# Kernel optimization log

Hardware: AMD Instinct MI355X
Metric: run time of the kernel (lower is better)

Reference implementation:

```python
import jax, jax.numpy as jnp
import numpy as np

_DIMS = [15, 30, 60, 90, 120, 90, 60, 30, 15, 10, 5, 1]


def setup_inputs() -> dict:
    key = jax.random.key(0)
    keys = jax.random.split(key, 1 + 2 * 11)
    inp = {"x": jax.random.normal(keys[0], (524288, 15), dtype=jnp.float32)}
    for i in range(11):
        fan_in, fan_out = _DIMS[i], _DIMS[i + 1]
        bound = 1.0 / np.sqrt(fan_in)
        inp[f"W{i+1}"] = jax.random.uniform(keys[1 + 2 * i], (fan_out, fan_in), minval=-bound, maxval=bound, dtype=jnp.float32)
        inp[f"b{i+1}"] = jax.random.uniform(keys[2 + 2 * i], (fan_out,), minval=-bound, maxval=bound, dtype=jnp.float32)
    return inp


def reference(x, W1, b1, W2, b2, W3, b3, W4, b4, W5, b5, W6, b6, W7, b7, W8, b8, W9, b9, W10, b10, W11, b11):
    Ws = [W1, W2, W3, W4, W5, W6, W7, W8, W9, W10, W11]
    bs = [b1, b2, b3, b4, b5, b6, b7, b8, b9, b10, b11]
    h = x
    # 10 Linear+ReLU layers, funnel 15->30->60->90->120->90->60->30->15->10->5
    for W, b in zip(Ws[:-1], bs[:-1]):
        h = jax.nn.relu(h @ W.T + b)
    # final Linear 5->1 + sigmoid
    return jax.nn.sigmoid(h @ Ws[-1].T + bs[-1])
```

## Files before the change

### kernel.cpp

```cpp
#include <hip/hip_runtime.h>
#include <math.h>


using bf16x8 = __attribute__((ext_vector_type(8))) short;
using f32x4  = __attribute__((ext_vector_type(4))) float;
using u16x8  = __attribute__((ext_vector_type(8))) unsigned short;
using u32x2  = __attribute__((ext_vector_type(2))) unsigned;
using u32x4  = __attribute__((ext_vector_type(4))) unsigned;
typedef __bf16 bf16x2_t __attribute__((ext_vector_type(2)));

namespace {
constexpr int NL = 11;
constexpr int IN_[NL]  = {15, 30, 60, 90, 120, 90, 60, 30, 15, 10, 5};
constexpr int OUT_[NL] = {30, 60, 90, 120, 90, 60, 30, 15, 10, 5, 1};
constexpr int KP_[NL]  = {32, 32, 64, 96, 128, 96, 64, 32, 32, 32, 32};
constexpr int NP_[NL]  = {32, 64, 96, 128, 96, 64, 32, 16, 16, 16, 16};
constexpr int E0 = 0;
constexpr int E1 = 1024;
constexpr int E2 = 5120;
constexpr int E3 = 11264;
constexpr int E4 = 19456;
constexpr int E5 = 25600;
constexpr int LDS_SHORTS = 29696;
constexpr int LDS_BYTES  = LDS_SHORTS * 2;
constexpr int G = 32;
}

__device__ __forceinline__ unsigned short f2bf(float f) {
    unsigned u = __float_as_uint(f);
    u += 0x7fffu + ((u >> 16) & 1u);
    return (unsigned short)(u >> 16);
}

__device__ __forceinline__ unsigned pk2(float a, float b) {
#if __has_builtin(__builtin_amdgcn_cvt_pk_bf16_f32)
    return __builtin_bit_cast(unsigned, __builtin_amdgcn_cvt_pk_bf16_f32(a, b));
#else
    bf16x2_t c;
    c[0] = (__bf16)a;
    c[1] = (__bf16)b;
    return __builtin_bit_cast(unsigned, c);
#endif
}

__device__ __forceinline__ u32x2 packrelu(f32x4 a) {
    u32x2 p;
    p[0] = pk2(fmaxf(a[0], 0.f), fmaxf(a[1], 0.f));
    p[1] = pk2(fmaxf(a[2], 0.f), fmaxf(a[3], 0.f));
    return p;
}

__device__ __forceinline__ bf16x8 xform(u32x2 pa, u32x2 pb, bool sel, int sA, int sB) {
    int a0 = __shfl((int)pa[0], sA);
    int b0 = __shfl((int)pb[0], sA);
    int a1 = __shfl((int)pa[1], sA);
    int b1 = __shfl((int)pb[1], sA);
    int a2 = __shfl((int)pa[0], sB);
    int b2 = __shfl((int)pb[0], sB);
    int a3 = __shfl((int)pa[1], sB);
    int b3 = __shfl((int)pb[1], sB);
    u32x4 r;
    r[0] = (unsigned)(sel ? b0 : a0);
    r[1] = (unsigned)(sel ? b1 : a1);
    r[2] = (unsigned)(sel ? b2 : a2);
    r[3] = (unsigned)(sel ? b3 : a3);
    return __builtin_bit_cast(bf16x8, r);
}

__device__ __forceinline__ bf16x8 xform16(u32x2 p, int quad, int sA16, int sB16) {
    int d0 = __shfl((int)p[0], sA16);
    int d1 = __shfl((int)p[1], sA16);
    int d2 = __shfl((int)p[0], sB16);
    int d3 = __shfl((int)p[1], sB16);
    u32x4 r;
    if (quad < 2) {
        r[0] = (unsigned)d0; r[1] = (unsigned)d1;
        r[2] = (unsigned)d2; r[3] = (unsigned)d3;
    } else {
        r[0] = (quad == 2) ? 0x00003F80u : 0u;
        r[1] = 0u; r[2] = 0u; r[3] = 0u;
    }
    return __builtin_bit_cast(bf16x8, r);
}

template <int L>
__device__ __forceinline__ void stage_w(const float* __restrict__ W,
                                        const float* __restrict__ B,
                                        short* s, int tid) {
    constexpr int KP = KP_[L], NP = NP_[L], INl = IN_[L], OUTl = OUT_[L];
    constexpr int NKT = KP / 32;
    for (int idx = tid; idx < NP * KP; idx += 512) {
        const int f    = idx >> 9;
        const int t    = idx & 511;
        const int quad = t >> 7;
        const int colc = (t >> 3) & 15;
        const int j    = t & 7;
        const int mt   = f / NKT;
        const int kt   = f - mt * NKT;
        const int m    = mt * 16 + colc;
        const int k    = kt * 32 + quad * 8 + j;
        float v = 0.f;
        if (m < OUTl) {
            if (k < INl) v = W[m * INl + k];
            else if (k == INl) v = B[m];
            else if (k == INl + 1) {
                float hf = __builtin_bit_cast(float, (unsigned)f2bf(B[m]) << 16);
                v = B[m] - hf;
            }
        } else if (m == OUTl || m == OUTl + 1) {
            if (k == INl) v = 1.f;
        }
        s[idx] = (short)f2bf(v);
    }
}

__device__ __forceinline__ bf16x8 ldfrag(const short* p) { return *(const bf16x8*)p; }

__device__ __forceinline__ void edge_write(short* tile, int mt, int col, int quad, f32x4 a) {
    const int wb = (mt >> 1) * 512 + ((mt & 1) * 2 + (quad >> 1)) * 128 + col * 8 + (quad & 1) * 4;
    *(u32x2*)(tile + wb) = packrelu(a);
}

__device__ __forceinline__ float4 ld4(const float* p) {
    float4 t;
    __builtin_memcpy(&t, p, 16);
    return t;
}

__device__ __forceinline__ void fetch_x2(const float* __restrict__ x, int row0,
                                         int col, int quad, float4 (&xv)[2]) {
#pragma unroll
    for (int t = 0; t < 2; ++t) {
        const float* xr = x + (long)(row0 + t * 16 + col) * 15;
        if (quad < 3) {
            xv[t] = ld4(xr + quad * 4);
        } else {
            float4 u = ld4(xr + 11);
            xv[t] = make_float4(u.y, u.z, u.w, 1.f);
        }
    }
}

extern "C" __global__ void __launch_bounds__(512, 4)
mlp_pipe(const float* __restrict__ x,
         const float* __restrict__ W0,  const float* __restrict__ B0,
         const float* __restrict__ W1,  const float* __restrict__ B1,
         const float* __restrict__ W2,  const float* __restrict__ B2,
         const float* __restrict__ W3,  const float* __restrict__ B3,
         const float* __restrict__ W4,  const float* __restrict__ B4,
         const float* __restrict__ W5,  const float* __restrict__ B5,
         const float* __restrict__ W6,  const float* __restrict__ B6,
         const float* __restrict__ W7,  const float* __restrict__ B7,
         const float* __restrict__ W8,  const float* __restrict__ B8,
         const float* __restrict__ W9,  const float* __restrict__ B9,
         const float* __restrict__ W10, const float* __restrict__ B10,
         float* __restrict__ out, int ng) {
    extern __shared__ __align__(16) short smem[];
    const int tid  = threadIdx.x;
    const int wave = tid >> 6;
    const int lane = tid & 63;
    const int col  = lane & 15;
    const int quad = lane >> 4;
    const int fo   = quad * 128 + col * 8;
    const bool sel = quad >= 2;
    const int sA   = col + 16 * (2 * (quad & 1));
    const int sB   = sA + 16;
    const int sA16 = col + 32 * (quad & 1);
    const int sB16 = sA16 + 16;

    bf16x8 wreg[12];
#pragma unroll
    for (int f = 0; f < 12; ++f) wreg[f] = bf16x8{0,0,0,0,0,0,0,0};

    stage_w<0>(W0, B0, smem, tid); __syncthreads();
    if (wave == 0) { wreg[0] = ldfrag(smem + fo); wreg[1] = ldfrag(smem + 512 + fo); }
    __syncthreads();
    stage_w<1>(W1, B1, smem, tid); __syncthreads();
    if (wave == 0) {
#pragma unroll
        for (int f = 0; f < 4; ++f) wreg[2 + f] = ldfrag(smem + f * 512 + fo);
    }
    __syncthreads();
    stage_w<2>(W2, B2, smem, tid); __syncthreads();
    if (wave == 1) {
#pragma unroll
        for (int f = 0; f < 12; ++f) wreg[f] = ldfrag(smem + f * 512 + fo);
    }
    __syncthreads();
    stage_w<3>(W3, B3, smem, tid); __syncthreads();
    if (wave == 2) {
#pragma unroll
        for (int f = 0; f < 12; ++f) wreg[f] = ldfrag(smem + f * 512 + fo);
    }
    if (wave == 3) {
#pragma unroll
        for (int f = 0; f < 12; ++f) wreg[f] = ldfrag(smem + (12 + f) * 512 + fo);
    }
    __syncthreads();
    stage_w<4>(W4, B4, smem, tid); __syncthreads();
    if (wave == 4) {
#pragma unroll
        for (int f = 0; f < 12; ++f) wreg[f] = ldfrag(smem + f * 512 + fo);
    }
    if (wave == 5) {
#pragma unroll
        for (int f = 0; f < 12; ++f) wreg[f] = ldfrag(smem + (12 + f) * 512 + fo);
    }
    __syncthreads();
    stage_w<5>(W5, B5, smem, tid); __syncthreads();
    if (wave == 6) {
#pragma unroll
        for (int f = 0; f < 12; ++f) wreg[f] = ldfrag(smem + f * 512 + fo);
    }
    __syncthreads();
    stage_w<6>(W6, B6, smem, tid); __syncthreads();
    if (wave == 7) {
#pragma unroll
        for (int f = 0; f < 4; ++f) wreg[f] = ldfrag(smem + f * 512 + fo);
    }
    __syncthreads();
    stage_w<7>(W7, B7, smem, tid); __syncthreads();
    if (wave == 7) wreg[4] = ldfrag(smem + fo);
    __syncthreads();
    stage_w<8>(W8, B8, smem, tid); __syncthreads();
    if (wave == 7) wreg[5] = ldfrag(smem + fo);
    __syncthreads();
    stage_w<9>(W9, B9, smem, tid); __syncthreads();
    if (wave == 7) wreg[6] = ldfrag(smem + fo);
    __syncthreads();
    stage_w<10>(W10, B10, smem, tid); __syncthreads();
    if (wave == 7) wreg[7] = ldfrag(smem + fo);
    __syncthreads();

    const int gbase = blockIdx.x * ng;
    float4 xv[2];
    if (wave == 0 && ng > 0) fetch_x2(x, gbase * G, col, quad, xv);

    for (int n = 0; n < ng + 5; ++n) {
        if (wave == 0) {
            const int g = n;
            if (g < ng) {
                short* sx = smem + E0;
                const int off = (quad >> 1) * 128 + col * 8 + (quad & 1) * 4;
#pragma unroll
                for (int t = 0; t < 2; ++t) {
                    u32x2 o;
                    o[0] = pk2(xv[t].x, xv[t].y);
                    o[1] = pk2(xv[t].z, xv[t].w);
                    *(u32x2*)(sx + t * 512 + off) = o;
                }
                u16x8 z = {0, 0, 0, 0, 0, 0, 0, 0};
                if (!(quad & 1)) z[0] = (unsigned short)0x3F80;
                *(u16x8*)(sx + (quad >> 1) * 512 + (2 + (quad & 1)) * 128 + col * 8) = z;

                if (g + 1 < ng) fetch_x2(x, (gbase + g + 1) * G, col, quad, xv);

                short* e1p = smem + E1 + (g & 1) * 2048;
#pragma unroll
                for (int t = 0; t < 2; ++t) {
                    bf16x8 xb = ldfrag(sx + t * 512 + fo);
                    f32x4 a0 = {0.f, 0.f, 0.f, 0.f}, a1 = {0.f, 0.f, 0.f, 0.f};
                    a0 = __builtin_amdgcn_mfma_f32_16x16x32_bf16(wreg[0], xb, a0, 0, 0, 0);
                    a1 = __builtin_amdgcn_mfma_f32_16x16x32_bf16(wreg[1], xb, a1, 0, 0, 0);
                    bf16x8 h1 = xform(packrelu(a0), packrelu(a1), sel, sA, sB);
                    f32x4 c[4];
#pragma unroll
                    for (int mt = 0; mt < 4; ++mt) c[mt] = f32x4{0.f, 0.f, 0.f, 0.f};
#pragma unroll
                    for (int mt = 0; mt < 4; ++mt)
                        c[mt] = __builtin_amdgcn_mfma_f32_16x16x32_bf16(wreg[2 + mt], h1, c[mt], 0, 0, 0);
#pragma unroll
                    for (int mt = 0; mt < 4; ++mt)
                        edge_write(e1p + t * 1024, mt, col, quad, c[mt]);
                }
            }
        } else if (wave == 1) {
            const int g = n - 1;
            if (g >= 0 && g < ng) {
                const short* e1p = smem + E1 + (g & 1) * 2048;
                short* e2p = smem + E2 + (g & 1) * 3072;
#pragma unroll
                for (int t = 0; t < 2; ++t) {
                    bf16x8 b0 = ldfrag(e1p + t * 1024 + fo);
                    bf16x8 b1 = ldfrag(e1p + t * 1024 + 512 + fo);
                    f32x4 acc[6];
#pragma unroll
                    for (int mt = 0; mt < 6; ++mt) acc[mt] = f32x4{0.f, 0.f, 0.f, 0.f};
#pragma unroll
                    for (int mt = 0; mt < 6; ++mt)
                        acc[mt] = __builtin_amdgcn_mfma_f32_16x16x32_bf16(wreg[mt * 2], b0, acc[mt], 0, 0, 0);
#pragma unroll
                    for (int mt = 0; mt < 6; ++mt)
                        acc[mt] = __builtin_amdgcn_mfma_f32_16x16x32_bf16(wreg[mt * 2 + 1], b1, acc[mt], 0, 0, 0);
#pragma unroll
                    for (int mt = 0; mt < 6; ++mt)
                        edge_write(e2p + t * 1536, mt, col, quad, acc[mt]);
                }
            }
        } else if (wave == 2 || wave == 3) {
            const int g = n - 2;
            if (g >= 0 && g < ng) {
                const short* e2p = smem + E2 + (g & 1) * 3072;
                short* e3p = smem + E3 + (g & 1) * 4096;
                const int mo = (wave == 3) ? 4 : 0;
                f32x4 acc[4][2];
#pragma unroll
                for (int mt = 0; mt < 4; ++mt)
#pragma unroll
                    for (int t = 0; t < 2; ++t) acc[mt][t] = f32x4{0.f, 0.f, 0.f, 0.f};
#pragma unroll
                for (int kt = 0; kt < 3; ++kt) {
                    bf16x8 q0 = ldfrag(e2p + kt * 512 + fo);
                    bf16x8 q1 = ldfrag(e2p + 1536 + kt * 512 + fo);
#pragma unroll
                    for (int mt = 0; mt < 4; ++mt) {
                        acc[mt][0] = __builtin_amdgcn_mfma_f32_16x16x32_bf16(wreg[mt * 3 + kt], q0, acc[mt][0], 0, 0, 0);
                        acc[mt][1] = __builtin_amdgcn_mfma_f32_16x16x32_bf16(wreg[mt * 3 + kt], q1, acc[mt][1], 0, 0, 0);
                    }
                }
#pragma unroll
                for (int mt = 0; mt < 4; ++mt)
#pragma unroll
                    for (int t = 0; t < 2; ++t)
                        edge_write(e3p + t * 2048, mo + mt, col, quad, acc[mt][t]);
            }
        } else if (wave == 4 || wave == 5) {
            const int g = n - 3;
            if (g >= 0 && g < ng) {
                const short* e3p = smem + E3 + (g & 1) * 4096;
                short* e4p = smem + E4 + (g & 1) * 3072;
                const int mo = (wave == 5) ? 3 : 0;
                f32x4 acc[3][2];
#pragma unroll
                for (int mt = 0; mt < 3; ++mt)
#pragma unroll
                    for (int t = 0; t < 2; ++t) acc[mt][t] = f32x4{0.f, 0.f, 0.f, 0.f};
#pragma unroll
                for (int kt = 0; kt < 4; ++kt) {
                    bf16x8 q0 = ldfrag(e3p + kt * 512 + fo);
                    bf16x8 q1 = ldfrag(e3p + 2048 + kt * 512 + fo);
#pragma unroll
                    for (int mt = 0; mt < 3; ++mt) {
                        const int f = mt * 4 + kt + ((wave == 5) ? 12 - 12 : 0);
                        acc[mt][0] = __builtin_amdgcn_mfma_f32_16x16x32_bf16(wreg[f], q0, acc[mt][0], 0, 0, 0);
                        acc[mt][1] = __builtin_amdgcn_mfma_f32_16x16x32_bf16(wreg[f], q1, acc[mt][1], 0, 0, 0);
                    }
                }
#pragma unroll
                for (int mt = 0; mt < 3; ++mt)
#pragma unroll
                    for (int t = 0; t < 2; ++t)
                        edge_write(e4p + t * 1536, mo + mt, col, quad, acc[mt][t]);
            }
        } else if (wave == 6) {
            const int g = n - 4;
            if (g >= 0 && g < ng) {
                const short* e4p = smem + E4 + (g & 1) * 3072;
                short* e5p = smem + E5 + (g & 1) * 2048;
                f32x4 acc[4][2];
#pragma unroll
                for (int mt = 0; mt < 4; ++mt)
#pragma unroll
                    for (int t = 0; t < 2; ++t) acc[mt][t] = f32x4{0.f, 0.f, 0.f, 0.f};
#pragma unroll
                for (int kt = 0; kt < 3; ++kt) {
                    bf16x8 q0 = ldfrag(e4p + kt * 512 + fo);
                    bf16x8 q1 = ldfrag(e4p + 1536 + kt * 512 + fo);
#pragma unroll
                    for (int mt = 0; mt < 4; ++mt) {
                        acc[mt][0] = __builtin_amdgcn_mfma_f32_16x16x32_bf16(wreg[mt * 3 + kt], q0, acc[mt][0], 0, 0, 0);
                        acc[mt][1] = __builtin_amdgcn_mfma_f32_16x16x32_bf16(wreg[mt * 3 + kt], q1, acc[mt][1], 0, 0, 0);
                    }
                }
#pragma unroll
                for (int mt = 0; mt < 4; ++mt)
#pragma unroll
                    for (int t = 0; t < 2; ++t)
                        edge_write(e5p + t * 1024, mt, col, quad, acc[mt][t]);
            }
        } else {
            const int g = n - 5;
            if (g >= 0 && g < ng) {
                const short* e5p = smem + E5 + (g & 1) * 2048;
#pragma unroll
                for (int t = 0; t < 2; ++t) {
                    bf16x8 b0 = ldfrag(e5p + t * 1024 + fo);
                    bf16x8 b1 = ldfrag(e5p + t * 1024 + 512 + fo);
                    f32x4 c0 = {0.f, 0.f, 0.f, 0.f}, c1 = {0.f, 0.f, 0.f, 0.f};
                    c0 = __builtin_amdgcn_mfma_f32_16x16x32_bf16(wreg[0], b0, c0, 0, 0, 0);
                    c0 = __builtin_amdgcn_mfma_f32_16x16x32_bf16(wreg[1], b1, c0, 0, 0, 0);
                    c1 = __builtin_amdgcn_mfma_f32_16x16x32_bf16(wreg[2], b0, c1, 0, 0, 0);
                    c1 = __builtin_amdgcn_mfma_f32_16x16x32_bf16(wreg[3], b1, c1, 0, 0, 0);
                    bf16x8 h7 = xform(packrelu(c0), packrelu(c1), sel, sA, sB);
                    f32x4 d = {0.f, 0.f, 0.f, 0.f};
                    d = __builtin_amdgcn_mfma_f32_16x16x32_bf16(wreg[4], h7, d, 0, 0, 0);
                    bf16x8 h8 = xform16(packrelu(d), quad, sA16, sB16);
                    f32x4 e = {0.f, 0.f, 0.f, 0.f};
                    e = __builtin_amdgcn_mfma_f32_16x16x32_bf16(wreg[5], h8, e, 0, 0, 0);
                    bf16x8 h9 = xform16(packrelu(e), quad, sA16, sB16);
                    f32x4 ff = {0.f, 0.f, 0.f, 0.f};
                    ff = __builtin_amdgcn_mfma_f32_16x16x32_bf16(wreg[6], h9, ff, 0, 0, 0);
                    bf16x8 h10 = xform16(packrelu(ff), quad, sA16, sB16);
                    f32x4 o = {0.f, 0.f, 0.f, 0.f};
                    o = __builtin_amdgcn_mfma_f32_16x16x32_bf16(wreg[7], h10, o, 0, 0, 0);
                    if (quad == 0)
                        out[(gbase + g) * G + t * 16 + col] = 1.f / (1.f + __expf(-o[0]));
                }
            }
        }
        __syncthreads();
    }
}

extern "C" void kernel_launch(void* const* d_in, const int* in_sizes, int n_in,
                              void* d_out, int out_size, void* d_ws, size_t ws_size,
                              hipStream_t stream) {
    (void)n_in; (void)d_ws; (void)ws_size; (void)out_size;
    const float* x = (const float*)d_in[0];
    const float* W[11];
    const float* B[11];
    for (int i = 0; i < 11; ++i) {
        W[i] = (const float*)d_in[1 + 2 * i];
        B[i] = (const float*)d_in[2 + 2 * i];
    }
    const int nrows  = in_sizes[0] / 15;
    const int blocks = 512;
    const int ng     = (nrows / G) / blocks;

    hipFuncSetAttribute((const void*)mlp_pipe,
                        hipFuncAttributeMaxDynamicSharedMemorySize, LDS_BYTES);

    mlp_pipe<<<dim3(blocks), dim3(512), LDS_BYTES, stream>>>(
        x,
        W[0], B[0], W[1], B[1], W[2], B[2], W[3], B[3], W[4], B[4],
        W[5], B[5], W[6], B[6], W[7], B[7], W[8], B[8], W[9], B[9],
        W[10], B[10],
        (float*)d_out, ng);
}
```

Measured before the change: 212.6 us.

## Use 16x16x16 MFMA for small layers, drop shuffles, move x fetch to last wave

Narrow layers (first two and last four) now use the 16x16x16 bf16 MFMA, so activations go straight from the accumulator layout into the next B operand, with no cross-lane shuffle transforms. The x prefetch and conversion move from wave 0 to wave 7, which writes a double-buffered bf16 x tile in LDS one group ahead. Weight staging is consolidated into two phases with fewer barriers, and the launch bound changes from 4 to 2 blocks per CU. The aim is to shorten the critical first and last pipeline stages. The cost is extra LDS traffic for x and possible register or occupancy shifts.

After: 209.0 us. Within noise of the previous version (-1.7%).

```diff
diff --git a/kernel.cpp b/kernel.cpp
--- a/kernel.cpp
+++ b/kernel.cpp
@@ -3,10 +3,9 @@
 
 
 using bf16x8 = __attribute__((ext_vector_type(8))) short;
+using s16x4  = __attribute__((ext_vector_type(4))) short;
 using f32x4  = __attribute__((ext_vector_type(4))) float;
-using u16x8  = __attribute__((ext_vector_type(8))) unsigned short;
 using u32x2  = __attribute__((ext_vector_type(2))) unsigned;
-using u32x4  = __attribute__((ext_vector_type(4))) unsigned;
 typedef __bf16 bf16x2_t __attribute__((ext_vector_type(2)));
 
 namespace {
@@ -15,14 +14,17 @@
 constexpr int OUT_[NL] = {30, 60, 90, 120, 90, 60, 30, 15, 10, 5, 1};
 constexpr int KP_[NL]  = {32, 32, 64, 96, 128, 96, 64, 32, 32, 32, 32};
 constexpr int NP_[NL]  = {32, 64, 96, 128, 96, 64, 32, 16, 16, 16, 16};
-constexpr int E0 = 0;
-constexpr int E1 = 1024;
-constexpr int E2 = 5120;
-constexpr int E3 = 11264;
-constexpr int E4 = 19456;
-constexpr int E5 = 25600;
+constexpr int E1 = 0;
+constexpr int E2 = 4096;
+constexpr int E3 = 10240;
+constexpr int E4 = 18432;
+constexpr int E5 = 24576;
+constexpr int E6 = 28672;
 constexpr int LDS_SHORTS = 29696;
 constexpr int LDS_BYTES  = LDS_SHORTS * 2;
+constexpr int S_L0 = 0, S_L1 = 512, S_L2 = 2560, S_L3 = 8704;
+constexpr int S_L7 = 20992, S_L8 = 21504, S_L9 = 21760, S_L10 = 22016;
+constexpr int S_L4 = 0, S_L5 = 12288, S_L6 = 18432;
 constexpr int G = 32;
 }
 
@@ -33,12 +35,10 @@
 }
 
 __device__ __forceinline__ unsigned pk2(float a, float b) {
-#if __has_builtin(__builtin_amdgcn_cvt_pk_bf16_f32)
+#if defined(__HIP_DEVICE_COMPILE__) && __has_builtin(__builtin_amdgcn_cvt_pk_bf16_f32)
     return __builtin_bit_cast(unsigned, __builtin_amdgcn_cvt_pk_bf16_f32(a, b));
 #else
-    bf16x2_t c;
-    c[0] = (__bf16)a;
-    c[1] = (__bf16)b;
+    bf16x2_t c; c[0] = (__bf16)a; c[1] = (__bf16)b;
     return __builtin_bit_cast(unsigned, c);
 #endif
 }
@@ -49,44 +49,41 @@
     p[1] = pk2(fmaxf(a[2], 0.f), fmaxf(a[3], 0.f));
     return p;
 }
-
-__device__ __forceinline__ bf16x8 xform(u32x2 pa, u32x2 pb, bool sel, int sA, int sB) {
-    int a0 = __shfl((int)pa[0], sA);
-    int b0 = __shfl((int)pb[0], sA);
-    int a1 = __shfl((int)pa[1], sA);
-    int b1 = __shfl((int)pb[1], sA);
-    int a2 = __shfl((int)pa[0], sB);
-    int b2 = __shfl((int)pb[0], sB);
-    int a3 = __shfl((int)pa[1], sB);
-    int b3 = __shfl((int)pb[1], sB);
-    u32x4 r;
-    r[0] = (unsigned)(sel ? b0 : a0);
-    r[1] = (unsigned)(sel ? b1 : a1);
-    r[2] = (unsigned)(sel ? b2 : a2);
-    r[3] = (unsigned)(sel ? b3 : a3);
-    return __builtin_bit_cast(bf16x8, r);
-}
-
-__device__ __forceinline__ bf16x8 xform16(u32x2 p, int quad, int sA16, int sB16) {
-    int d0 = __shfl((int)p[0], sA16);
-    int d1 = __shfl((int)p[1], sA16);
-    int d2 = __shfl((int)p[0], sB16);
-    int d3 = __shfl((int)p[1], sB16);
-    u32x4 r;
-    if (quad < 2) {
-        r[0] = (unsigned)d0; r[1] = (unsigned)d1;
-        r[2] = (unsigned)d2; r[3] = (unsigned)d3;
-    } else {
-        r[0] = (quad == 2) ? 0x00003F80u : 0u;
-        r[1] = 0u; r[2] = 0u; r[3] = 0u;
-    }
-    return __builtin_bit_cast(bf16x8, r);
+__device__ __forceinline__ s16x4 pr16(f32x4 a) {
+    return __builtin_bit_cast(s16x4, packrelu(a));
+}
+
+__device__ __forceinline__ f32x4 mfma32(bf16x8 a, bf16x8 b, f32x4 c) {
+    return __builtin_amdgcn_mfma_f32_16x16x32_bf16(a, b, c, 0, 0, 0);
+}
+
+__device__ __forceinline__ s16x4 lo8(bf16x8 v) { return __builtin_shufflevector(v, v, 0, 1, 2, 3); }
+__device__ __forceinline__ s16x4 hi8(bf16x8 v) { return __builtin_shufflevector(v, v, 4, 5, 6, 7); }
+__device__ __forceinline__ bf16x8 cat4(s16x4 a, s16x4 b) { return __builtin_shufflevector(a, b, 0, 1, 2, 3, 4, 5, 6, 7); }
+
+__device__ __forceinline__ f32x4 mfma16(s16x4 a, s16x4 b, f32x4 c) {
+#if defined(__HIP_DEVICE_COMPILE__) && __has_builtin(__builtin_amdgcn_mfma_f32_16x16x16bf16_1k)
+    return __builtin_amdgcn_mfma_f32_16x16x16bf16_1k(a, b, c, 0, 0, 0);
+#else
+    const s16x4 z = {0, 0, 0, 0};
+    return mfma32(cat4(a, z), cat4(b, z), c);
+#endif
+}
+
+__device__ __forceinline__ bf16x8 ldfrag(const short* p) { return *(const bf16x8*)p; }
+__device__ __forceinline__ s16x4 ld16(const short* base, int f, int quad, int col) {
+    return *(const s16x4*)(base + f * 256 + quad * 64 + col * 4);
+}
+
+__device__ __forceinline__ void edge_write(short* tile, int mt, int col, int quad, f32x4 a) {
+    const int wb = (mt >> 1) * 512 + ((mt & 1) * 2 + (quad >> 1)) * 128 + col * 8 + (quad & 1) * 4;
+    *(u32x2*)(tile + wb) = packrelu(a);
 }
 
 template <int L>
 __device__ __forceinline__ void stage_w(const float* __restrict__ W,
                                         const float* __restrict__ B,
-                                        short* s, int tid) {
+                                        short* dst, int tid) {
     constexpr int KP = KP_[L], NP = NP_[L], INl = IN_[L], OUTl = OUT_[L];
     constexpr int NKT = KP / 32;
     for (int idx = tid; idx < NP * KP; idx += 512) {
@@ -110,21 +107,42 @@
         } else if (m == OUTl || m == OUTl + 1) {
             if (k == INl) v = 1.f;
         }
-        s[idx] = (short)f2bf(v);
-    }
-}
-
-__device__ __forceinline__ bf16x8 ldfrag(const short* p) { return *(const bf16x8*)p; }
-
-__device__ __forceinline__ void edge_write(short* tile, int mt, int col, int quad, f32x4 a) {
-    const int wb = (mt >> 1) * 512 + ((mt & 1) * 2 + (quad >> 1)) * 128 + col * 8 + (quad & 1) * 4;
-    *(u32x2*)(tile + wb) = packrelu(a);
+        dst[idx] = (short)f2bf(v);
+    }
+}
+
+template <int INl, int OUTl, int KP16, int NP, bool BLO, int NGEN>
+__device__ __forceinline__ void stage_w16(const float* __restrict__ W,
+                                          const float* __restrict__ B,
+                                          short* dst, int tid) {
+    for (int idx = tid; idx < NP * KP16; idx += 512) {
+        const int f    = idx >> 8;
+        const int t    = idx & 255;
+        const int quad = t >> 6;
+        const int colc = (t >> 2) & 15;
+        const int j    = t & 3;
+        constexpr int NKT = KP16 / 16;
+        const int mt   = f / NKT;
+        const int kt   = f - mt * NKT;
+        const int m    = mt * 16 + colc;
+        const int k    = kt * 16 + quad * 4 + j;
+        float v = 0.f;
+        if (m < OUTl) {
+            if (k < INl) v = W[m * INl + k];
+            else if (k == INl) v = B[m];
+            else if (BLO && k == INl + 1) {
+                float hf = __builtin_bit_cast(float, (unsigned)f2bf(B[m]) << 16);
+                v = B[m] - hf;
+            }
+        } else if (m < OUTl + NGEN) {
+            if (k == INl) v = 1.f;
+        }
+        dst[idx] = (short)f2bf(v);
+    }
 }
 
 __device__ __forceinline__ float4 ld4(const float* p) {
-    float4 t;
-    __builtin_memcpy(&t, p, 16);
-    return t;
+    float4 t; __builtin_memcpy(&t, p, 16); return t;
 }
 
 __device__ __forceinline__ void fetch_x2(const float* __restrict__ x, int row0,
@@ -141,7 +159,7 @@
     }
 }
 
-extern "C" __global__ void __launch_bounds__(512, 4)
+extern "C" __global__ void __launch_bounds__(512, 2)
 mlp_pipe(const float* __restrict__ x,
          const float* __restrict__ W0,  const float* __restrict__ B0,
          const float* __restrict__ W1,  const float* __restrict__ B1,
@@ -157,124 +175,108 @@
          float* __restrict__ out, int ng) {
     extern __shared__ __align__(16) short smem[];
     const int tid  = threadIdx.x;
-    const int wave = tid >> 6;
     const int lane = tid & 63;
     const int col  = lane & 15;
     const int quad = lane >> 4;
     const int fo   = quad * 128 + col * 8;
-    const bool sel = quad >= 2;
-    const int sA   = col + 16 * (2 * (quad & 1));
-    const int sB   = sA + 16;
-    const int sA16 = col + 32 * (quad & 1);
-    const int sB16 = sA16 + 16;
-
-    bf16x8 wreg[12];
-#pragma unroll
-    for (int f = 0; f < 12; ++f) wreg[f] = bf16x8{0,0,0,0,0,0,0,0};
-
-    stage_w<0>(W0, B0, smem, tid); __syncthreads();
-    if (wave == 0) { wreg[0] = ldfrag(smem + fo); wreg[1] = ldfrag(smem + 512 + fo); }
+    const int sw   = __builtin_amdgcn_readfirstlane(tid >> 6);
+
+    bf16x8 wk[12];
+#pragma unroll
+    for (int f = 0; f < 12; ++f) wk[f] = bf16x8{0, 0, 0, 0, 0, 0, 0, 0};
+    s16x4 t7a{0,0,0,0}, t7b{0,0,0,0}, t8{0,0,0,0}, t9{0,0,0,0}, t10{0,0,0,0};
+
+    stage_w16<15, 30, 16, 32, false, 2>(W0, B0, smem + S_L0, tid);
+    stage_w16<30, 60, 32, 64, true,  2>(W1, B1, smem + S_L1, tid);
+    stage_w<2>(W2, B2, smem + S_L2, tid);
+    stage_w<3>(W3, B3, smem + S_L3, tid);
+    stage_w16<30, 15, 32, 16, true,  1>(W7, B7, smem + S_L7, tid);
+    stage_w16<15, 10, 16, 16, false, 2>(W8, B8, smem + S_L8, tid);
+    stage_w16<10,  5, 16, 16, true,  2>(W9, B9, smem + S_L9, tid);
+    stage_w16< 5,  1, 16, 16, true,  0>(W10, B10, smem + S_L10, tid);
     __syncthreads();
-    stage_w<1>(W1, B1, smem, tid); __syncthreads();
-    if (wave == 0) {
-#pragma unroll
-        for (int f = 0; f < 4; ++f) wreg[2 + f] = ldfrag(smem + f * 512 + fo);
+    if (sw == 0) {
+        wk[0] = cat4(ld16(smem + S_L0, 0, quad, col), ld16(smem + S_L0, 1, quad, col));
+#pragma unroll
+        for (int m = 0; m < 4; ++m)
+            wk[1 + m] = cat4(ld16(smem + S_L1, 2 * m, quad, col),
+                             ld16(smem + S_L1, 2 * m + 1, quad, col));
+    } else if (sw == 1) {
+#pragma unroll
+        for (int f = 0; f < 12; ++f) wk[f] = ldfrag(smem + S_L2 + f * 512 + fo);
+    } else if (sw == 2) {
+#pragma unroll
+        for (int f = 0; f < 12; ++f) wk[f] = ldfrag(smem + S_L3 + f * 512 + fo);
+    } else if (sw == 3) {
+#pragma unroll
+        for (int f = 0; f < 12; ++f) wk[f] = ldfrag(smem + S_L3 + (12 + f) * 512 + fo);
+    } else if (sw == 7) {
+        t7a = ld16(smem + S_L7, 0, quad, col);
+        t7b = ld16(smem + S_L7, 1, quad, col);
+        t8  = ld16(smem + S_L8, 0, quad, col);
+        t9  = ld16(smem + S_L9, 0, quad, col);
+        t10 = ld16(smem + S_L10, 0, quad, col);
     }
     __syncthreads();
-    stage_w<2>(W2, B2, smem, tid); __syncthreads();
-    if (wave == 1) {
-#pragma unroll
-        for (int f = 0; f < 12; ++f) wreg[f] = ldfrag(smem + f * 512 + fo);
-    }
+    stage_w<4>(W4, B4, smem + S_L4, tid);
+    stage_w<5>(W5, B5, smem + S_L5, tid);
+    stage_w<6>(W6, B6, smem + S_L6, tid);
     __syncthreads();
-    stage_w<3>(W3, B3, smem, tid); __syncthreads();
-    if (wave == 2) {
-#pragma unroll
-        for (int f = 0; f < 12; ++f) wreg[f] = ldfrag(smem + f * 512 + fo);
-    }
-    if (wave == 3) {
-#pragma unroll
-        for (int f = 0; f < 12; ++f) wreg[f] = ldfrag(smem + (12 + f) * 512 + fo);
+    if (sw == 4) {
+#pragma unroll
+        for (int f = 0; f < 12; ++f) wk[f] = ldfrag(smem + S_L4 + f * 512 + fo);
+    } else if (sw == 5) {
+#pragma unroll
+        for (int f = 0; f < 12; ++f) wk[f] = ldfrag(smem + S_L4 + (12 + f) * 512 + fo);
+    } else if (sw == 6) {
+#pragma unroll
+        for (int f = 0; f < 12; ++f) wk[f] = ldfrag(smem + S_L5 + f * 512 + fo);
+    } else if (sw == 7) {
+#pragma unroll
+        for (int f = 0; f < 4; ++f) wk[f] = ldfrag(smem + S_L6 + f * 512 + fo);
     }
     __syncthreads();
-    stage_w<4>(W4, B4, smem, tid); __syncthreads();
-    if (wave == 4) {
-#pragma unroll
-        for (int f = 0; f < 12; ++f) wreg[f] = ldfrag(smem + f * 512 + fo);
-    }
-    if (wave == 5) {
-#pragma unroll
-        for (int f = 0; f < 12; ++f) wreg[f] = ldfrag(smem + (12 + f) * 512 + fo);
+
+    const int gbase = blockIdx.x * ng;
+
+    if (sw == 7 && ng > 0) {
+        float4 xf[2];
+        fetch_x2(x, gbase * G, col, quad, xf);
+#pragma unroll
+        for (int t = 0; t < 2; ++t) {
+            u32x2 o; o[0] = pk2(xf[t].x, xf[t].y); o[1] = pk2(xf[t].z, xf[t].w);
+            *(s16x4*)(smem + E6 + t * 256 + quad * 64 + col * 4) = __builtin_bit_cast(s16x4, o);
+        }
     }
     __syncthreads();
-    stage_w<5>(W5, B5, smem, tid); __syncthreads();
-    if (wave == 6) {
-#pragma unroll
-        for (int f = 0; f < 12; ++f) wreg[f] = ldfrag(smem + f * 512 + fo);
-    }
-    __syncthreads();
-    stage_w<6>(W6, B6, smem, tid); __syncthreads();
-    if (wave == 7) {
-#pragma unroll
-        for (int f = 0; f < 4; ++f) wreg[f] = ldfrag(smem + f * 512 + fo);
-    }
-    __syncthreads();
-    stage_w<7>(W7, B7, smem, tid); __syncthreads();
-    if (wave == 7) wreg[4] = ldfrag(smem + fo);
-    __syncthreads();
-    stage_w<8>(W8, B8, smem, tid); __syncthreads();
-    if (wave == 7) wreg[5] = ldfrag(smem + fo);
-    __syncthreads();
-    stage_w<9>(W9, B9, smem, tid); __syncthreads();
-    if (wave == 7) wreg[6] = ldfrag(smem + fo);
-    __syncthreads();
-    stage_w<10>(W10, B10, smem, tid); __syncthreads();
-    if (wave == 7) wreg[7] = ldfrag(smem + fo);
-    __syncthreads();
-
-    const int gbase = blockIdx.x * ng;
-    float4 xv[2];
-    if (wave == 0 && ng > 0) fetch_x2(x, gbase * G, col, quad, xv);
 
     for (int n = 0; n < ng + 5; ++n) {
-        if (wave == 0) {
+        if (sw == 0) {
             const int g = n;
             if (g < ng) {
-                short* sx = smem + E0;
-                const int off = (quad >> 1) * 128 + col * 8 + (quad & 1) * 4;
+                const short* xe = smem + E6 + (g & 1) * 512;
+                short* e1p = smem + E1 + (g & 1) * 2048;
 #pragma unroll
                 for (int t = 0; t < 2; ++t) {
-                    u32x2 o;
-                    o[0] = pk2(xv[t].x, xv[t].y);
-                    o[1] = pk2(xv[t].z, xv[t].w);
-                    *(u32x2*)(sx + t * 512 + off) = o;
-                }
-                u16x8 z = {0, 0, 0, 0, 0, 0, 0, 0};
-                if (!(quad & 1)) z[0] = (unsigned short)0x3F80;
-                *(u16x8*)(sx + (quad >> 1) * 512 + (2 + (quad & 1)) * 128 + col * 8) = z;
-
-                if (g + 1 < ng) fetch_x2(x, (gbase + g + 1) * G, col, quad, xv);
-
-                short* e1p = smem + E1 + (g & 1) * 2048;
-#pragma unroll
-                for (int t = 0; t < 2; ++t) {
-                    bf16x8 xb = ldfrag(sx + t * 512 + fo);
-                    f32x4 a0 = {0.f, 0.f, 0.f, 0.f}, a1 = {0.f, 0.f, 0.f, 0.f};
-                    a0 = __builtin_amdgcn_mfma_f32_16x16x32_bf16(wreg[0], xb, a0, 0, 0, 0);
-                    a1 = __builtin_amdgcn_mfma_f32_16x16x32_bf16(wreg[1], xb, a1, 0, 0, 0);
-                    bf16x8 h1 = xform(packrelu(a0), packrelu(a1), sel, sA, sB);
-                    f32x4 c[4];
-#pragma unroll
-                    for (int mt = 0; mt < 4; ++mt) c[mt] = f32x4{0.f, 0.f, 0.f, 0.f};
+                    s16x4 xb = *(const s16x4*)(xe + t * 256 + quad * 64 + col * 4);
+                    f32x4 c0{0.f,0.f,0.f,0.f}, c1{0.f,0.f,0.f,0.f};
+                    c0 = mfma16(lo8(wk[0]), xb, c0);
+                    c1 = mfma16(hi8(wk[0]), xb, c1);
+                    s16x4 h1a = pr16(c0), h1b = pr16(c1);
+                    f32x4 d[4];
+#pragma unroll
+                    for (int mt = 0; mt < 4; ++mt) d[mt] = f32x4{0.f,0.f,0.f,0.f};
+#pragma unroll
+                    for (int mt = 0; mt < 4; ++mt) {
+                        d[mt] = mfma16(lo8(wk[1 + mt]), h1a, d[mt]);
+                        d[mt] = mfma16(hi8(wk[1 + mt]), h1b, d[mt]);
+                    }
 #pragma unroll
                     for (int mt = 0; mt < 4; ++mt)
-                        c[mt] = __builtin_amdgcn_mfma_f32_16x16x32_bf16(wreg[2 + mt], h1, c[mt], 0, 0, 0);
-#pragma unroll
-                    for (int mt = 0; mt < 4; ++mt)
-                        edge_write(e1p + t * 1024, mt, col, quad, c[mt]);
-                }
-            }
-        } else if (wave == 1) {
+                        edge_write(e1p + t * 1024, mt, col, quad, d[mt]);
+                }
+            }
+        } else if (sw == 1) {
             const int g = n - 1;
             if (g >= 0 && g < ng) {
                 const short* e1p = smem + E1 + (g & 1) * 2048;
@@ -285,37 +287,36 @@
                     bf16x8 b1 = ldfrag(e1p + t * 1024 + 512 + fo);
                     f32x4 acc[6];
 #pragma unroll
-                    for (int mt = 0; mt < 6; ++mt) acc[mt] = f32x4{0.f, 0.f, 0.f, 0.f};
-#pragma unroll
-                    for (int mt = 0; mt < 6; ++mt)
-                        acc[mt] = __builtin_amdgcn_mfma_f32_16x16x32_bf16(wreg[mt * 2], b0, acc[mt], 0, 0, 0);
-#pragma unroll
-                    for (int mt = 0; mt < 6; ++mt)
-                        acc[mt] = __builtin_amdgcn_mfma_f32_16x16x32_bf16(wreg[mt * 2 + 1], b1, acc[mt], 0, 0, 0);
+                    for (int mt = 0; mt < 6; ++mt) acc[mt] = f32x4{0.f,0.f,0.f,0.f};
+#pragma unroll
+                    for (int mt = 0; mt < 6; ++mt) {
+                        acc[mt] = mfma32(wk[2 * mt], b0, acc[mt]);
+                        acc[mt] = mfma32(wk[2 * mt + 1], b1, acc[mt]);
+                    }
 #pragma unroll
                     for (int mt = 0; mt < 6; ++mt)
                         edge_write(e2p + t * 1536, mt, col, quad, acc[mt]);
                 }
             }
-        } else if (wave == 2 || wave == 3) {
+        } else if (sw == 2 || sw == 3) {
             const int g = n - 2;
             if (g >= 0 && g < ng) {
                 const short* e2p = smem + E2 + (g & 1) * 3072;
                 short* e3p = smem + E3 + (g & 1) * 4096;
-                const int mo = (wave == 3) ? 4 : 0;
+                const int mo = (sw == 3) ? 4 : 0;
                 f32x4 acc[4][2];
 #pragma unroll
                 for (int mt = 0; mt < 4; ++mt)
 #pragma unroll
-                    for (int t = 0; t < 2; ++t) acc[mt][t] = f32x4{0.f, 0.f, 0.f, 0.f};
+                    for (int t = 0; t < 2; ++t) acc[mt][t] = f32x4{0.f,0.f,0.f,0.f};
 #pragma unroll
                 for (int kt = 0; kt < 3; ++kt) {
                     bf16x8 q0 = ldfrag(e2p + kt * 512 + fo);
                     bf16x8 q1 = ldfrag(e2p + 1536 + kt * 512 + fo);
 #pragma unroll
                     for (int mt = 0; mt < 4; ++mt) {
-                        acc[mt][0] = __builtin_amdgcn_mfma_f32_16x16x32_bf16(wreg[mt * 3 + kt], q0, acc[mt][0], 0, 0, 0);
-                        acc[mt][1] = __builtin_amdgcn_mfma_f32_16x16x32_bf16(wreg[mt * 3 + kt], q1, acc[mt][1], 0, 0, 0);
+                        acc[mt][0] = mfma32(wk[mt * 3 + kt], q0, acc[mt][0]);
+                        acc[mt][1] = mfma32(wk[mt * 3 + kt], q1, acc[mt][1]);
                     }
                 }
 #pragma unroll
@@ -324,26 +325,25 @@
                     for (int t = 0; t < 2; ++t)
                         edge_write(e3p + t * 2048, mo + mt, col, quad, acc[mt][t]);
             }
-        } else if (wave == 4 || wave == 5) {
+        } else if (sw == 4 || sw == 5) {
             const int g = n - 3;
             if (g >= 0 && g < ng) {
                 const short* e3p = smem + E3 + (g & 1) * 4096;
                 short* e4p = smem + E4 + (g & 1) * 3072;
-                const int mo = (wave == 5) ? 3 : 0;
+                const int mo = (sw == 5) ? 3 : 0;
                 f32x4 acc[3][2];
 #pragma unroll
                 for (int mt = 0; mt < 3; ++mt)
 #pragma unroll
-                    for (int t = 0; t < 2; ++t) acc[mt][t] = f32x4{0.f, 0.f, 0.f, 0.f};
+                    for (int t = 0; t < 2; ++t) acc[mt][t] = f32x4{0.f,0.f,0.f,0.f};
 #pragma unroll
                 for (int kt = 0; kt < 4; ++kt) {
                     bf16x8 q0 = ldfrag(e3p + kt * 512 + fo);
                     bf16x8 q1 = ldfrag(e3p + 2048 + kt * 512 + fo);
 #pragma unroll
                     for (int mt = 0; mt < 3; ++mt) {
-                        const int f = mt * 4 + kt + ((wave == 5) ? 12 - 12 : 0);
-                        acc[mt][0] = __builtin_amdgcn_mfma_f32_16x16x32_bf16(wreg[f], q0, acc[mt][0], 0, 0, 0);
-                        acc[mt][1] = __builtin_amdgcn_mfma_f32_16x16x32_bf16(wreg[f], q1, acc[mt][1], 0, 0, 0);
+                        acc[mt][0] = mfma32(wk[mt * 4 + kt], q0, acc[mt][0]);
+                        acc[mt][1] = mfma32(wk[mt * 4 + kt], q1, acc[mt][1]);
                     }
                 }
 #pragma unroll
@@ -352,7 +352,7 @@
                     for (int t = 0; t < 2; ++t)
                         edge_write(e4p + t * 1536, mo + mt, col, quad, acc[mt][t]);
             }
-        } else if (wave == 6) {
+        } else if (sw == 6) {
             const int g = n - 4;
             if (g >= 0 && g < ng) {
                 const short* e4p = smem + E4 + (g & 1) * 3072;
@@ -361,15 +361,15 @@
 #pragma unroll
                 for (int mt = 0; mt < 4; ++mt)
 #pragma unroll
-                    for (int t = 0; t < 2; ++t) acc[mt][t] = f32x4{0.f, 0.f, 0.f, 0.f};
+                    for (int t = 0; t < 2; ++t) acc[mt][t] = f32x4{0.f,0.f,0.f,0.f};
 #pragma unroll
                 for (int kt = 0; kt < 3; ++kt) {
                     bf16x8 q0 = ldfrag(e4p + kt * 512 + fo);
                     bf16x8 q1 = ldfrag(e4p + 1536 + kt * 512 + fo);
 #pragma unroll
                     for (int mt = 0; mt < 4; ++mt) {
-                        acc[mt][0] = __builtin_amdgcn_mfma_f32_16x16x32_bf16(wreg[mt * 3 + kt], q0, acc[mt][0], 0, 0, 0);
-                        acc[mt][1] = __builtin_amdgcn_mfma_f32_16x16x32_bf16(wreg[mt * 3 + kt], q1, acc[mt][1], 0, 0, 0);
+                        acc[mt][0] = mfma32(wk[mt * 3 + kt], q0, acc[mt][0]);
+                        acc[mt][1] = mfma32(wk[mt * 3 + kt], q1, acc[mt][1]);
                     }
                 }
 #pragma unroll
@@ -379,6 +379,9 @@
                         edge_write(e5p + t * 1024, mt, col, quad, acc[mt][t]);
             }
         } else {
+            const int gx = n + 1;
+            float4 xf[2];
+            if (gx < ng) fetch_x2(x, (gbase + gx) * G, col, quad, xf);
             const int g = n - 5;
             if (g >= 0 && g < ng) {
                 const short* e5p = smem + E5 + (g & 1) * 2048;
@@ -386,25 +389,34 @@
                 for (int t = 0; t < 2; ++t) {
                     bf16x8 b0 = ldfrag(e5p + t * 1024 + fo);
                     bf16x8 b1 = ldfrag(e5p + t * 1024 + 512 + fo);
-                    f32x4 c0 = {0.f, 0.f, 0.f, 0.f}, c1 = {0.f, 0.f, 0.f, 0.f};
-                    c0 = __builtin_amdgcn_mfma_f32_16x16x32_bf16(wreg[0], b0, c0, 0, 0, 0);
-                    c0 = __builtin_amdgcn_mfma_f32_16x16x32_bf16(wreg[1], b1, c0, 0, 0, 0);
-                    c1 = __builtin_amdgcn_mfma_f32_16x16x32_bf16(wreg[2], b0, c1, 0, 0, 0);
-                    c1 = __builtin_amdgcn_mfma_f32_16x16x32_bf16(wreg[3], b1, c1, 0, 0, 0);
-                    bf16x8 h7 = xform(packrelu(c0), packrelu(c1), sel, sA, sB);
-                    f32x4 d = {0.f, 0.f, 0.f, 0.f};
-                    d = __builtin_amdgcn_mfma_f32_16x16x32_bf16(wreg[4], h7, d, 0, 0, 0);
-                    bf16x8 h8 = xform16(packrelu(d), quad, sA16, sB16);
-                    f32x4 e = {0.f, 0.f, 0.f, 0.f};
-                    e = __builtin_amdgcn_mfma_f32_16x16x32_bf16(wreg[5], h8, e, 0, 0, 0);
-                    bf16x8 h9 = xform16(packrelu(e), quad, sA16, sB16);
-                    f32x4 ff = {0.f, 0.f, 0.f, 0.f};
-                    ff = __builtin_amdgcn_mfma_f32_16x16x32_bf16(wreg[6], h9, ff, 0, 0, 0);
-                    bf16x8 h10 = xform16(packrelu(ff), quad, sA16, sB16);
-                    f32x4 o = {0.f, 0.f, 0.f, 0.f};
-                    o = __builtin_amdgcn_mfma_f32_16x16x32_bf16(wreg[7], h10, o, 0, 0, 0);
+                    f32x4 c0{0.f,0.f,0.f,0.f}, c1{0.f,0.f,0.f,0.f};
+                    c0 = mfma32(wk[0], b0, c0);
+                    c0 = mfma32(wk[1], b1, c0);
+                    c1 = mfma32(wk[2], b0, c1);
+                    c1 = mfma32(wk[3], b1, c1);
+                    s16x4 h7a = pr16(c0), h7b = pr16(c1);
+                    f32x4 d{0.f,0.f,0.f,0.f};
+                    d = mfma16(t7a, h7a, d);
+                    d = mfma16(t7b, h7b, d);
+                    s16x4 h8 = pr16(d);
+                    f32x4 e{0.f,0.f,0.f,0.f};
+                    e = mfma16(t8, h8, e);
+                    s16x4 h9 = pr16(e);
+                    f32x4 f4{0.f,0.f,0.f,0.f};
+                    f4 = mfma16(t9, h9, f4);
+                    s16x4 h10 = pr16(f4);
+                    f32x4 o{0.f,0.f,0.f,0.f};
+                    o = mfma16(t10, h10, o);
                     if (quad == 0)
                         out[(gbase + g) * G + t * 16 + col] = 1.f / (1.f + __expf(-o[0]));
+                }
+            }
+            if (gx < ng) {
+#pragma unroll
+                for (int t = 0; t < 2; ++t) {
+                    u32x2 o; o[0] = pk2(xf[t].x, xf[t].y); o[1] = pk2(xf[t].z, xf[t].w);
+                    *(s16x4*)(smem + E6 + (gx & 1) * 512 + t * 256 + quad * 64 + col * 4) =
+                        __builtin_bit_cast(s16x4, o);
                 }
             }
         }
@@ -425,10 +437,7 @@
     }
     const int nrows  = in_sizes[0] / 15;
     const int blocks = 512;
-    const int ng     = (nrows / G) / blocks;
-
-    hipFuncSetAttribute((const void*)mlp_pipe,
-                        hipFuncAttributeMaxDynamicSharedMemorySize, LDS_BYTES);
+    const int ng     = nrows / (blocks * G);
 
     mlp_pipe<<<dim3(blocks), dim3(512), LDS_BYTES, stream>>>(
         x,
```
